# Optimization experiments

Measured on AMD Instinct MI355X. Metric: run time of the kernel, lower is better.

The kernel has to match this reference:

```python
import jax, jax.numpy as jnp
import numpy as np

EMBED = 1024
HEADS = 16
HEAD_DIM = EMBED // HEADS
B, T = 2, 2048


def setup_inputs() -> dict:
    key = jax.random.key(0)
    k1, k2, k3, k4, k5 = jax.random.split(key, 5)
    x = jax.random.normal(k1, (B, T, EMBED), dtype=jnp.float32)
    Wq = jax.random.normal(k2, (HEADS, EMBED, HEAD_DIM), dtype=jnp.float32)
    Wk = jax.random.normal(k3, (HEADS, EMBED, HEAD_DIM), dtype=jnp.float32)
    Wv = jax.random.normal(k4, (HEADS, EMBED, HEAD_DIM), dtype=jnp.float32)
    # nn.Linear weight is [out_features, in_features]
    Wo = jax.random.normal(k5, (EMBED, EMBED), dtype=jnp.float32) * (1.0 / np.sqrt(EMBED))
    return {"x": x, "Wq": Wq, "Wk": Wk, "Wv": Wv, "Wo": Wo}


def reference(x, Wq, Wk, Wv, Wo):
    b, t, e = x.shape
    h, _, i = Wq.shape
    q = jnp.einsum('hei,bte->hbti', Wq, x)
    k = jnp.einsum('hei,bte->hbti', Wk, x)
    v = jnp.einsum('hei,bte->hbti', Wv, x)
    # NOTE: original module scales by sqrt(seq_len), not sqrt(head_dim)
    fit = jnp.einsum('hbti,hbsi->hbts', q, k) / jnp.sqrt(jnp.float32(t))
    fit = jax.nn.softmax(fit, axis=-1)
    attended = jnp.einsum('hbts,hbsi->hbti', fit, v)
    # rearrange 'h b t i -> b t (h i)'
    attended = attended.transpose(1, 2, 0, 3).reshape(b, t, h * i)
    return attended @ Wo.T
```

## Files before the change

### kernel.cpp

```cpp
#include <hip/hip_runtime.h>
#include <math.h>

#define E_DIM 1024
#define H_NUM 16
#define HD 64
#define B_NUM 2
#define T_LEN 2048

typedef unsigned short u16;
typedef short bf16x8 __attribute__((ext_vector_type(8)));
typedef float f32x4 __attribute__((ext_vector_type(4)));
typedef unsigned short u16x4 __attribute__((ext_vector_type(4)));
typedef unsigned short u16x8 __attribute__((ext_vector_type(8)));
typedef unsigned int u32x2 __attribute__((ext_vector_type(2)));

#define MFMA16(a, b, c) __builtin_amdgcn_mfma_f32_16x16x32_bf16(a, b, c, 0, 0, 0)

__device__ __forceinline__ u16 f2bf(float f) {
    unsigned u = __float_as_uint(f);
    u += 0x7FFFu + ((u >> 16) & 1u);
    return (u16)(u >> 16);
}
__device__ __forceinline__ float bf2f(u16 b) {
    return __uint_as_float(((unsigned)b) << 16);
}
__device__ __forceinline__ void gl_lds16(const void* g, void* l) {
    __builtin_amdgcn_global_load_lds(
        (const __attribute__((address_space(1))) unsigned int*)g,
        (__attribute__((address_space(3))) unsigned int*)l, 16, 0, 0);
}


__global__ __launch_bounds__(256) void convert_all_kernel(
    const float* __restrict__ x,
    const float* __restrict__ Wq, const float* __restrict__ Wk, const float* __restrict__ Wv,
    const float* __restrict__ Wo,
    u16* __restrict__ xh, u16* __restrict__ xl,
    u16* __restrict__ wtp_h, u16* __restrict__ wtp_l,
    u16* __restrict__ wop)
{
    const int bid = blockIdx.x;
    const int tid = threadIdx.x;

    if (bid < 4096) {
        int i = (bid * 256 + tid) * 4;
        float4 f = *(const float4*)&x[i];
        float fv[4] = {f.x, f.y, f.z, f.w};
        u16x4 h, l;
        #pragma unroll
        for (int j = 0; j < 4; j++) {
            u16 hi = f2bf(fv[j]);
            h[j] = hi;
            l[j] = f2bf(fv[j] - bf2f(hi));
        }
        *(u16x4*)&xh[i] = h;
        *(u16x4*)&xl[i] = l;
    } else if (bid < 4096 + 768) {
        const int bx = bid - 4096;
        const int m = bx >> 8, h = (bx >> 4) & 15, e0 = (bx & 15) * 64;
        const float* W = (m == 0 ? Wq : (m == 1 ? Wk : Wv));

        __shared__ u16 Th[64][65];
        __shared__ u16 Tl[64][65];

        #pragma unroll
        for (int j = 0; j < 16; j++) {
            int idx = j * 256 + tid;
            int e = idx >> 6, i = idx & 63;
            float f = W[((size_t)h * E_DIM + e0 + e) * HD + i];
            u16 hi = f2bf(f);
            Th[i][e] = hi;
            Tl[i][e] = f2bf(f - bf2f(hi));
        }
        __syncthreads();
        #pragma unroll
        for (int rep = 0; rep < 2; rep++) {
            int c = rep * 256 + tid;
            int ct_loc = c >> 7, ke_loc = (c >> 6) & 1, lane = c & 63;
            int col = ct_loc * 16 + (lane & 15);
            int el  = ke_loc * 32 + (lane >> 4) * 8;
            int ct_g = m * 64 + h * 4 + ct_loc;
            int ke_g = (bx & 15) * 2 + ke_loc;
            size_t off = ((size_t)ct_g * 32 + ke_g) * 512 + (size_t)lane * 8;
            *(u16x8*)&wtp_h[off] = *(u16x8*)&Th[col][el];
            *(u16x8*)&wtp_l[off] = *(u16x8*)&Tl[col][el];
        }
    } else {
        int c = (bid - 4096 - 768) * 256 + tid;
        int lane = c & 63, ke = (c >> 6) & 31, ct = c >> 11;
        int row = ct * 16 + (lane & 15);
        int e   = ke * 32 + (lane >> 4) * 8;
        const float* src = &Wo[(size_t)row * E_DIM + e];
        float4 f0 = *(const float4*)&src[0];
        float4 f1 = *(const float4*)&src[4];
        float fv[8] = {f0.x, f0.y, f0.z, f0.w, f1.x, f1.y, f1.z, f1.w};
        u16x8 hv;
        #pragma unroll
        for (int j = 0; j < 8; j++) hv[j] = f2bf(fv[j]);
        *(u16x8*)&wop[(size_t)c * 8] = hv;
    }
}

__global__ __launch_bounds__(256, 3) void qkv_mfma_kernel(
    const u16* __restrict__ xh, const u16* __restrict__ xl,
    const u16* __restrict__ wtp_h, const u16* __restrict__ wtp_l,
    u16* __restrict__ qp_h, u16* __restrict__ qp_l,
    u16* __restrict__ kp_h, u16* __restrict__ kp_l,
    u16* __restrict__ vp)
{
    const int bx = blockIdx.x;
    const int r0 = blockIdx.y * 128;
    const int m  = bx >> 3;
    const bool lo = (m != 2);

    __shared__ __align__(16) u16 SM[17408];
    u16* Ah = SM;
    u16* Al = SM + 4096;
    u16* Bh = SM + 8192;
    u16* Bl = SM + 12288;

    const int tid = threadIdx.x;
    const int w = tid >> 6, lane = tid & 63;
    const int qd = lane >> 4, n16 = lane & 15;
    const int wr = w >> 1, wc = w & 1;

    f32x4 acc[4][4];
    #pragma unroll
    for (int i = 0; i < 4; i++)
        #pragma unroll
        for (int j = 0; j < 4; j++) acc[i][j] = (f32x4){0.f, 0.f, 0.f, 0.f};

    for (int k0 = 0; k0 < E_DIM; k0 += 32) {
        __syncthreads();
        const int ke = k0 >> 5;
        #pragma unroll
        for (int rep = 0; rep < 2; rep++) {
            int c = rep * 256 + tid;
            int mt = c >> 6;
            int cl = c & 63;
            int cn = cl & 15, cq = cl >> 4;
            size_t aoff = (size_t)(r0 + mt * 16 + cn) * E_DIM + k0 + cq * 8;
            gl_lds16(&xh[aoff], &Ah[c * 8]);
            if (lo) gl_lds16(&xl[aoff], &Al[c * 8]);
        }
        #pragma unroll
        for (int rep = 0; rep < 2; rep++) {
            int c = rep * 256 + tid;
            int ct_loc = c >> 6;
            int cl = c & 63;
            size_t boff = ((size_t)(bx * 8 + ct_loc) * 32 + ke) * 512 + (size_t)cl * 8;
            gl_lds16(&wtp_h[boff], &Bh[c * 8]);
            if (lo) gl_lds16(&wtp_l[boff], &Bl[c * 8]);
        }
        __syncthreads();

        bf16x8 ah[4], al_[4];
        #pragma unroll
        for (int i = 0; i < 4; i++) {
            ah[i] = *(bf16x8*)&Ah[((wr * 4 + i) * 64 + lane) * 8];
            if (lo) al_[i] = *(bf16x8*)&Al[((wr * 4 + i) * 64 + lane) * 8];
        }
        #pragma unroll
        for (int j = 0; j < 4; j++) {
            bf16x8 bh = *(bf16x8*)&Bh[((wc * 4 + j) * 64 + lane) * 8];
            if (lo) {
                bf16x8 bl = *(bf16x8*)&Bl[((wc * 4 + j) * 64 + lane) * 8];
                #pragma unroll
                for (int i = 0; i < 4; i++) {
                    acc[i][j] = MFMA16(ah[i], bh, acc[i][j]);
                    acc[i][j] = MFMA16(al_[i], bh, acc[i][j]);
                    acc[i][j] = MFMA16(ah[i], bl, acc[i][j]);
                }
            } else {
                #pragma unroll
                for (int i = 0; i < 4; i++)
                    acc[i][j] = MFMA16(ah[i], bh, acc[i][j]);
            }
        }
    }

    const int b  = r0 >> 11;
    const int tloc0 = r0 & 2047;

    if (m == 2) {
        const int h0 = (bx & 7) * 2;
        __syncthreads();
        const int VS = 136;
        u16* TR = SM + wc * 8704;
        #pragma unroll
        for (int i = 0; i < 4; i++) {
            int tl = wr * 64 + i * 16 + qd * 4;
            #pragma unroll
            for (int j = 0; j < 4; j++) {
                int d = j * 16 + n16;
                u16x4 pv;
                #pragma unroll
                for (int r = 0; r < 4; r++) pv[r] = f2bf(acc[i][j][r]);
                *(u16x4*)&TR[d * VS + tl] = pv;
            }
        }
        __syncthreads();
        const int st_g0 = tloc0 >> 6;
        #pragma unroll
        for (int rep = 0; rep < 8; rep++) {
            int c = rep * 256 + tid;
            int hh = c >> 10;
            int idx = c & 1023;
            int st_loc = idx >> 9, ks = (idx >> 8) & 1, dt = (idx >> 6) & 3, cl = idx & 63;
            int d  = dt * 16 + (cl & 15);
            int tl = st_loc * 64 + ks * 32 + (cl >> 4) * 8;
            u16x8 v8 = *(u16x8*)&SM[hh * 8704 + d * VS + tl];
            int hbv = (h0 + hh) * 2 + b;
            size_t off = ((((size_t)hbv * 32 + st_g0 + st_loc) * 2 + ks) * 4 + dt) * 512
                       + (size_t)cl * 8;
            *(u16x8*)&vp[off] = v8;
        }
    } else {
        const int h0 = (bx & 7) * 2;
        const float sc = (m == 0) ? 0.031882937f : 1.0f;
        u16* oh = (m == 0) ? qp_h : kp_h;
        u16* ol = (m == 0) ? qp_l : kp_l;
        const int hb = (h0 + wc) * 2 + b;
        #pragma unroll
        for (int i = 0; i < 4; i++) {
            int nt = (tloc0 >> 4) + wr * 4 + i;
            #pragma unroll
            for (int j = 0; j < 4; j++) {
                int ks = j >> 1;
                int lp = (((j & 1) * 2 + (n16 >> 3)) << 4);
                int pos = n16 & 7;
                size_t cb = (((size_t)hb * 128 + nt) * 2 + ks) * 512;
                #pragma unroll
                for (int r = 0; r < 4; r++) {
                    float f = acc[i][j][r] * sc;
                    u16 hi = f2bf(f);
                    size_t o = cb + (size_t)(lp | (qd * 4 + r)) * 8 + pos;
                    oh[o] = hi;
                    ol[o] = f2bf(f - bf2f(hi));
                }
            }
        }
    }
}

__global__ __launch_bounds__(256) void attn_kernel(
    const u16* __restrict__ qp_h, const u16* __restrict__ qp_l,
    const u16* __restrict__ kp_h, const u16* __restrict__ kp_l,
    const u16* __restrict__ vp, u16* __restrict__ attb)
{
    const int hb = blockIdx.x;
    const int h = hb >> 1, b = hb & 1;
    const int t0 = blockIdx.y * 64;

    __shared__ __align__(16) u16 BKh0[4096], BKl0[4096];
    __shared__ __align__(16) u16 BKh1[4096], BKl1[4096];
    __shared__ __align__(16) u16 PT[4][16][72];

    const int tid  = threadIdx.x;
    const int lane = tid & 63;
    const int w    = tid >> 6;
    const int qd   = lane >> 4;
    const int n16  = lane & 15;

    bf16x8 bqh[2], bql[2];
    {
        int qt = (t0 >> 4) + w;
        #pragma unroll
        for (int ks = 0; ks < 2; ks++) {
            size_t off = (((size_t)hb * 128 + qt) * 2 + ks) * 512 + (size_t)lane * 8;
            bqh[ks] = *(const bf16x8*)&qp_h[off];
            bql[ks] = *(const bf16x8*)&qp_l[off];
        }
    }

    f32x4 o4[4];
    #pragma unroll
    for (int dt = 0; dt < 4; dt++) o4[dt] = (f32x4){0.f, 0.f, 0.f, 0.f};
    float mr = -1e30f, lr = 0.f;

    {
        const size_t kb = (size_t)hb * 128 * 2 * 512;
        #pragma unroll
        for (int rep = 0; rep < 2; rep++) {
            int c = rep * 256 + tid;
            gl_lds16(&kp_h[kb + (size_t)c * 8], &BKh0[c * 8]);
            gl_lds16(&kp_l[kb + (size_t)c * 8], &BKl0[c * 8]);
        }
    }

    auto step = [&](int st, u16* RDh, u16* RDl, u16* WRh, u16* WRl) {
        __syncthreads();

        if (st + 1 < T_LEN / 64) {
            const size_t kb = ((size_t)hb * 128 + (st + 1) * 4) * 2 * 512;
            #pragma unroll
            for (int rep = 0; rep < 2; rep++) {
                int c = rep * 256 + tid;
                gl_lds16(&kp_h[kb + (size_t)c * 8], &WRh[c * 8]);
                gl_lds16(&kp_l[kb + (size_t)c * 8], &WRl[c * 8]);
            }
        }

        bf16x8 av[4][2];
        #pragma unroll
        for (int ks = 0; ks < 2; ks++)
            #pragma unroll
            for (int dt = 0; dt < 4; dt++) {
                size_t off = ((((size_t)hb * 32 + st) * 2 + ks) * 4 + dt) * 512
                           + (size_t)lane * 8;
                av[dt][ks] = *(const bf16x8*)&vp[off];
            }

        f32x4 s[4];
        #pragma unroll
        for (int c = 0; c < 4; c++) s[c] = (f32x4){0.f, 0.f, 0.f, 0.f};
        #pragma unroll
        for (int ks = 0; ks < 2; ks++) {
            #pragma unroll
            for (int c = 0; c < 4; c++) {
                bf16x8 akh = *(bf16x8*)&RDh[((c * 2 + ks) * 64 + lane) * 8];
                bf16x8 akl = *(bf16x8*)&RDl[((c * 2 + ks) * 64 + lane) * 8];
                s[c] = MFMA16(akh, bqh[ks], s[c]);
                s[c] = MFMA16(akh, bql[ks], s[c]);
                s[c] = MFMA16(akl, bqh[ks], s[c]);
            }
        }

        float tmax = s[0][0];
        #pragma unroll
        for (int c = 0; c < 4; c++)
            #pragma unroll
            for (int r = 0; r < 4; r++) tmax = fmaxf(tmax, s[c][r]);
        tmax = fmaxf(tmax, __shfl_xor(tmax, 16));
        tmax = fmaxf(tmax, __shfl_xor(tmax, 32));
        float nm = fmaxf(mr, tmax);
        float al = __builtin_amdgcn_exp2f(mr - nm);
        mr = nm;

        float psum = 0.f;
        #pragma unroll
        for (int c = 0; c < 4; c++) {
            float p0 = __builtin_amdgcn_exp2f(s[c][0] - nm);
            float p1 = __builtin_amdgcn_exp2f(s[c][1] - nm);
            float p2 = __builtin_amdgcn_exp2f(s[c][2] - nm);
            float p3 = __builtin_amdgcn_exp2f(s[c][3] - nm);
            psum += (p0 + p1) + (p2 + p3);
            u32x2 pk;
            pk[0] = (__float_as_uint(p0) >> 16) | (__float_as_uint(p1) & 0xFFFF0000u);
            pk[1] = (__float_as_uint(p2) >> 16) | (__float_as_uint(p3) & 0xFFFF0000u);
            *(u32x2*)&PT[w][n16][c * 16 + qd * 4] = pk;
        }
        if (__any(al != 1.0f)) {
            lr *= al;
            #pragma unroll
            for (int dt = 0; dt < 4; dt++)
                #pragma unroll
                for (int r = 0; r < 4; r++) o4[dt][r] *= al;
        }
        lr += psum;

        #pragma unroll
        for (int ks = 0; ks < 2; ks++) {
            bf16x8 bp = *(bf16x8*)&PT[w][n16][ks * 32 + qd * 8];
            #pragma unroll
            for (int dt = 0; dt < 4; dt++)
                o4[dt] = MFMA16(av[dt][ks], bp, o4[dt]);
        }
    };

    for (int i = 0; i < T_LEN / 128; i++) {
        step(2 * i,     BKh0, BKl0, BKh1, BKl1);
        step(2 * i + 1, BKh1, BKl1, BKh0, BKl0);
    }

    lr += __shfl_xor(lr, 16);
    lr += __shfl_xor(lr, 32);
    float inv = 1.f / lr;
    int row = t0 + w * 16 + n16;
    #pragma unroll
    for (int dt = 0; dt < 4; dt++) {
        u16x4 ov;
        #pragma unroll
        for (int r = 0; r < 4; r++) ov[r] = f2bf(o4[dt][r] * inv);
        *(u16x4*)&attb[(size_t)(b * T_LEN + row) * E_DIM + h * HD + dt * 16 + qd * 4] = ov;
    }
}

__global__ __launch_bounds__(256) void outproj_mfma_kernel(
    const u16* __restrict__ attb, const u16* __restrict__ wop,
    float* __restrict__ out)
{
    const int c0 = blockIdx.x * 64;
    const int r0 = blockIdx.y * 128;

    __shared__ __align__(16) u16 As[8192];

    const int tid = threadIdx.x;
    const int w = tid >> 6, lane = tid & 63;
    const int qd = lane >> 4, n16 = lane & 15;
    const int wr = w >> 1, wc = w & 1;

    f32x4 acc[4][2];
    #pragma unroll
    for (int i = 0; i < 4; i++)
        #pragma unroll
        for (int j = 0; j < 2; j++) acc[i][j] = (f32x4){0.f, 0.f, 0.f, 0.f};

    for (int k0 = 0; k0 < E_DIM; k0 += 64) {
        __syncthreads();
        #pragma unroll
        for (int rep = 0; rep < 4; rep++) {
            int c = rep * 256 + tid;
            int mt = c >> 7, ks = (c >> 6) & 1;
            int cl = c & 63;
            int cn = cl & 15, cq = cl >> 4;
            gl_lds16(&attb[(size_t)(r0 + mt * 16 + cn) * E_DIM + k0 + ks * 32 + cq * 8],
                     &As[c * 8]);
        }
        bf16x8 bb[2][2];
        #pragma unroll
        for (int j = 0; j < 2; j++) {
            int ct = (c0 >> 4) + wc * 2 + j;
            #pragma unroll
            for (int ks = 0; ks < 2; ks++) {
                int ke = (k0 >> 5) + ks;
                bb[j][ks] = *(const bf16x8*)&wop[((size_t)ct * 32 + ke) * 512 + (size_t)lane * 8];
            }
        }
        __syncthreads();

        #pragma unroll
        for (int ks = 0; ks < 2; ks++) {
            bf16x8 a[4];
            #pragma unroll
            for (int i = 0; i < 4; i++)
                a[i] = *(bf16x8*)&As[(((wr * 4 + i) * 2 + ks) * 64 + lane) * 8];
            #pragma unroll
            for (int j = 0; j < 2; j++)
                #pragma unroll
                for (int i = 0; i < 4; i++)
                    acc[i][j] = MFMA16(a[i], bb[j][ks], acc[i][j]);
        }
    }

    #pragma unroll
    for (int i = 0; i < 4; i++) {
        #pragma unroll
        for (int r = 0; r < 4; r++) {
            int row = r0 + wr * 64 + i * 16 + qd * 4 + r;
            #pragma unroll
            for (int j = 0; j < 2; j++) {
                int col = c0 + wc * 32 + j * 16 + n16;
                out[(size_t)row * E_DIM + col] = acc[i][j][r];
            }
        }
    }
}

extern "C" void kernel_launch(void* const* d_in, const int* in_sizes, int n_in,
                              void* d_out, int out_size, void* d_ws, size_t ws_size,
                              hipStream_t stream)
{
    const float* x  = (const float*)d_in[0];
    const float* Wq = (const float*)d_in[1];
    const float* Wk = (const float*)d_in[2];
    const float* Wv = (const float*)d_in[3];
    const float* Wo = (const float*)d_in[4];
    float* out = (float*)d_out;

    const size_t NX = (size_t)4096 * 1024;
    const size_t NW = (size_t)3072 * 1024;
    const size_t NO = (size_t)1024 * 1024;
    const size_t NQ = (size_t)H_NUM * B_NUM * T_LEN * HD;

    u16* xh   = (u16*)d_ws;
    u16* xl   = xh + NX;
    u16* wtph = xl + NX;
    u16* wtpl = wtph + NW;
    u16* wop  = wtpl + NW;
    u16* qph  = wop + NO;
    u16* qpl  = qph + NQ;
    u16* kph  = qpl + NQ;
    u16* kpl  = kph + NQ;
    u16* vp   = kpl + NQ;
    u16* attb = xh;

    convert_all_kernel<<<4096 + 768 + 512, 256, 0, stream>>>(
        x, Wq, Wk, Wv, Wo, xh, xl, wtph, wtpl, wop);

    dim3 g1(24, 32);
    qkv_mfma_kernel<<<g1, 256, 0, stream>>>(xh, xl, wtph, wtpl, qph, qpl, kph, kpl, vp);

    dim3 g2(H_NUM * B_NUM, T_LEN / 64);
    attn_kernel<<<g2, 256, 0, stream>>>(qph, qpl, kph, kpl, vp, attb);

    dim3 g3(E_DIM / 64, 4096 / 128);
    outproj_mfma_kernel<<<g3, 256, 0, stream>>>(attb, wop, out);
}
```

Before: 259.4 us.

## Load K tiles directly from global into registers instead of double-buffered LDS

Removes the double-buffered LDS staging of K (high/low bf16 halves) along with the per-step __syncthreads, and instead has each wave read its K fragments straight from global/L2 into registers. V loads are moved after the softmax, and launch bounds now request 3 blocks per CU. The aim is to cut LDS usage and block-wide barriers so occupancy rises. The cost is that every one of the 4 waves re-reads the same K tile from global memory, which adds L2 traffic and exposes load latency because there is no explicit prefetch.

Result: slower. 269.3 us (+3.8%).

```diff
diff --git a/kernel.cpp b/kernel.cpp
--- a/kernel.cpp
+++ b/kernel.cpp
@@ -243,7 +243,7 @@
     }
 }
 
-__global__ __launch_bounds__(256) void attn_kernel(
+__global__ __launch_bounds__(256, 3) void attn_kernel(
     const u16* __restrict__ qp_h, const u16* __restrict__ qp_l,
     const u16* __restrict__ kp_h, const u16* __restrict__ kp_l,
     const u16* __restrict__ vp, u16* __restrict__ attb)
@@ -252,8 +252,6 @@
     const int h = hb >> 1, b = hb & 1;
     const int t0 = blockIdx.y * 64;
 
-    __shared__ __align__(16) u16 BKh0[4096], BKl0[4096];
-    __shared__ __align__(16) u16 BKh1[4096], BKl1[4096];
     __shared__ __align__(16) u16 PT[4][16][72];
 
     const int tid  = threadIdx.x;
@@ -278,37 +276,16 @@
     for (int dt = 0; dt < 4; dt++) o4[dt] = (f32x4){0.f, 0.f, 0.f, 0.f};
     float mr = -1e30f, lr = 0.f;
 
-    {
-        const size_t kb = (size_t)hb * 128 * 2 * 512;
-        #pragma unroll
-        for (int rep = 0; rep < 2; rep++) {
-            int c = rep * 256 + tid;
-            gl_lds16(&kp_h[kb + (size_t)c * 8], &BKh0[c * 8]);
-            gl_lds16(&kp_l[kb + (size_t)c * 8], &BKl0[c * 8]);
-        }
-    }
-
-    auto step = [&](int st, u16* RDh, u16* RDl, u16* WRh, u16* WRl) {
-        __syncthreads();
-
-        if (st + 1 < T_LEN / 64) {
-            const size_t kb = ((size_t)hb * 128 + (st + 1) * 4) * 2 * 512;
-            #pragma unroll
-            for (int rep = 0; rep < 2; rep++) {
-                int c = rep * 256 + tid;
-                gl_lds16(&kp_h[kb + (size_t)c * 8], &WRh[c * 8]);
-                gl_lds16(&kp_l[kb + (size_t)c * 8], &WRl[c * 8]);
-            }
-        }
-
-        bf16x8 av[4][2];
+    for (int st = 0; st < T_LEN / 64; st++) {
+        const size_t kb = ((size_t)hb * 128 + st * 4) * 1024;
+        bf16x8 akh[2][4], akl[2][4];
         #pragma unroll
         for (int ks = 0; ks < 2; ks++)
             #pragma unroll
-            for (int dt = 0; dt < 4; dt++) {
-                size_t off = ((((size_t)hb * 32 + st) * 2 + ks) * 4 + dt) * 512
-                           + (size_t)lane * 8;
-                av[dt][ks] = *(const bf16x8*)&vp[off];
+            for (int c = 0; c < 4; c++) {
+                size_t o = kb + (size_t)((c * 2 + ks) * 64 + lane) * 8;
+                akh[ks][c] = *(const bf16x8*)&kp_h[o];
+                akl[ks][c] = *(const bf16x8*)&kp_l[o];
             }
 
         f32x4 s[4];
@@ -318,11 +295,9 @@
         for (int ks = 0; ks < 2; ks++) {
             #pragma unroll
             for (int c = 0; c < 4; c++) {
-                bf16x8 akh = *(bf16x8*)&RDh[((c * 2 + ks) * 64 + lane) * 8];
-                bf16x8 akl = *(bf16x8*)&RDl[((c * 2 + ks) * 64 + lane) * 8];
-                s[c] = MFMA16(akh, bqh[ks], s[c]);
-                s[c] = MFMA16(akh, bql[ks], s[c]);
-                s[c] = MFMA16(akl, bqh[ks], s[c]);
+                s[c] = MFMA16(akh[ks][c], bqh[ks], s[c]);
+                s[c] = MFMA16(akh[ks][c], bql[ks], s[c]);
+                s[c] = MFMA16(akl[ks][c], bqh[ks], s[c]);
             }
         }
 
@@ -359,6 +334,16 @@
         }
         lr += psum;
 
+        bf16x8 av[4][2];
+        #pragma unroll
+        for (int ks = 0; ks < 2; ks++)
+            #pragma unroll
+            for (int dt = 0; dt < 4; dt++) {
+                size_t off = ((((size_t)hb * 32 + st) * 2 + ks) * 4 + dt) * 512
+                           + (size_t)lane * 8;
+                av[dt][ks] = *(const bf16x8*)&vp[off];
+            }
+
         #pragma unroll
         for (int ks = 0; ks < 2; ks++) {
             bf16x8 bp = *(bf16x8*)&PT[w][n16][ks * 32 + qd * 8];
@@ -366,11 +351,6 @@
             for (int dt = 0; dt < 4; dt++)
                 o4[dt] = MFMA16(av[dt][ks], bp, o4[dt]);
         }
-    };
-
-    for (int i = 0; i < T_LEN / 128; i++) {
-        step(2 * i,     BKh0, BKl0, BKh1, BKl1);
-        step(2 * i + 1, BKh1, BKl1, BKh0, BKl0);
     }
 
     lr += __shfl_xor(lr, 16);
```
